# Optimization experiments

Measured on AMD Instinct MI355X. Metric: run time of the kernel, lower is better.

The kernel has to match this reference:

```python
import jax, jax.numpy as jnp
import numpy as np

B, N, C = 2, 2048, 1024
H = 16
HD = C // H
GH = C // 4  # spatial gate hidden dim


def setup_inputs() -> dict:
    key = jax.random.key(0)
    ks = jax.random.split(key, 10)
    s = 0.02
    return {
        "x": jax.random.normal(ks[0], (B, N, C), dtype=jnp.float32),
        "spatial_mask": jax.random.uniform(ks[1], (B, N), dtype=jnp.float32),
        # qkv Linear: weight [3C, C], bias [3C] (torch convention: y = x @ W.T + b)
        "qkv_w": jax.random.normal(ks[2], (3 * C, C), dtype=jnp.float32) * s,
        "qkv_b": jnp.zeros((3 * C,), dtype=jnp.float32),
        # output proj Linear: weight [C, C], bias [C]
        "proj_w": jax.random.normal(ks[3], (C, C), dtype=jnp.float32) * s,
        "proj_b": jnp.zeros((C,), dtype=jnp.float32),
        # spatial_gate: Linear(1, C//4) -> ReLU -> Linear(C//4, 1) -> Sigmoid
        "g1_w": jax.random.normal(ks[4], (GH, 1), dtype=jnp.float32) * 0.5,
        "g1_b": jnp.zeros((GH,), dtype=jnp.float32),
        "g2_w": jax.random.normal(ks[5], (1, GH), dtype=jnp.float32) * 0.1,
        "g2_b": jnp.zeros((1,), dtype=jnp.float32),
    }


def reference(x, spatial_mask, qkv_w, qkv_b, proj_w, proj_b, g1_w, g1_b, g2_w, g2_b):
    b, n, c = x.shape
    # QKV projection: [B, N, 3C] -> [3, B, H, N, HD]
    qkv = (x @ qkv_w.T + qkv_b).reshape(b, n, 3, H, HD).transpose(2, 0, 3, 1, 4)
    q, k, v = qkv[0], qkv[1], qkv[2]

    # scaled attention scores [B, H, N, N]
    attn = jnp.einsum("bhqd,bhkd->bhqk", q, k) * (HD ** -0.5)

    # spatial gate on the mask: scalar MLP applied per key position
    m = spatial_mask[..., None]                      # [B, N, 1]
    h = jax.nn.relu(m @ g1_w.T + g1_b)               # [B, N, GH]
    gate = jax.nn.sigmoid(h @ g2_w.T + g2_b)         # [B, N, 1]
    gate = gate[:, None, None, :, 0]                 # [B, 1, 1, N] broadcasts over heads & queries

    attn = jax.nn.softmax(attn * gate, axis=-1)

    out = jnp.einsum("bhqk,bhkd->bhqd", attn, v)     # [B, H, N, HD]
    out = out.transpose(0, 2, 1, 3).reshape(b, n, c) # [B, N, C]
    return out @ proj_w.T + proj_b
```

## Files before the change

### kernel.cpp

```cpp
#include <hip/hip_runtime.h>

#define H 16
#define NSEQ 2048
#define HD 64
#define CDIM 1024

typedef __attribute__((ext_vector_type(8))) short s8v;
typedef __attribute__((ext_vector_type(4))) float f4v;

#define GLL(g, l) __builtin_amdgcn_global_load_lds( \
    (const __attribute__((address_space(1))) void*)(g), \
    (__attribute__((address_space(3))) void*)(l), 16, 0, 0)

__device__ __forceinline__ short f2bf(float f) {
  union { float f; unsigned u; } x; x.f = f;
  unsigned r = (x.u + 0x7fffu + ((x.u >> 16) & 1u)) >> 16;
  return (short)r;
}

__global__ __launch_bounds__(256) void cvt_kernel(const float* __restrict__ in,
                                                  short* __restrict__ out, int n4) {
  int i = blockIdx.x * 256 + threadIdx.x;
  if (i < n4) {
    float4 f = ((const float4*)in)[i];
    short4 s;
    s.x = f2bf(f.x); s.y = f2bf(f.y); s.z = f2bf(f.z); s.w = f2bf(f.w);
    ((short4*)out)[i] = s;
  }
}

__global__ __launch_bounds__(256) void gate_kernel(const float* __restrict__ mask,
    const float* __restrict__ g1w, const float* __restrict__ g1b,
    const float* __restrict__ g2w, const float* __restrict__ g2b,
    float* __restrict__ gate) {
  int i = blockIdx.x * 256 + threadIdx.x;
  float m = mask[i];
  float acc = 0.f;
  for (int j = 0; j < 256; j++) {
    float h = m * g1w[j] + g1b[j];
    h = fmaxf(h, 0.f);
    acc += g2w[j] * h;
  }
  gate[i] = 1.f / (1.f + __expf(-(acc + g2b[0])));
}

__global__ __launch_bounds__(256) void gemm_qkv(const short* __restrict__ X,
    const short* __restrict__ W, const float* __restrict__ bias,
    short* __restrict__ qws, short* __restrict__ kws, short* __restrict__ vtws) {
  __shared__ __align__(16) short At[4096];
  __shared__ __align__(16) short Bt[4096];
  const int K = CDIM;
  int tid = threadIdx.x;
  int lane = tid & 63, w = tid >> 6;
  int quad = lane >> 4, l15 = lane & 15;
  int wm = w >> 1, wn = w & 1;
  long rowBase = (long)blockIdx.y * 128;
  long colBase = (long)blockIdx.x * 128;
  const f4v fz = {0.f, 0.f, 0.f, 0.f};
  f4v acc[4][4];
#pragma unroll
  for (int i = 0; i < 4; i++)
#pragma unroll
    for (int j = 0; j < 4; j++) acc[i][j] = fz;

  int j0 = tid, j1 = 256 + tid;
  int sr0 = j0 >> 2, sp0 = j0 & 3, sc0 = sp0 ^ ((sr0 >> 1) & 3);
  int sr1 = j1 >> 2, sp1 = j1 & 3, sc1 = sp1 ^ ((sr1 >> 1) & 3);
  const short* Xa = X + (rowBase + sr0) * K + sc0 * 8;
  const short* Xb = X + (rowBase + sr1) * K + sc1 * 8;
  const short* Wa = W + (colBase + sr0) * K + sc0 * 8;
  const short* Wb = W + (colBase + sr1) * K + sc1 * 8;

  for (int k0 = 0; k0 < K; k0 += 32) {
    __syncthreads();
    GLL(Xa + k0, &At[j0 * 8]);
    GLL(Xb + k0, &At[j1 * 8]);
    GLL(Wa + k0, &Bt[j0 * 8]);
    GLL(Wb + k0, &Bt[j1 * 8]);
    __syncthreads();
    s8v a[4], b[4];
#pragma unroll
    for (int mi = 0; mi < 4; mi++) {
      int row = wm * 64 + mi * 16 + l15;
      a[mi] = *(const s8v*)&At[row * 32 + ((quad ^ ((row >> 1) & 3)) * 8)];
    }
#pragma unroll
    for (int ni = 0; ni < 4; ni++) {
      int row = wn * 64 + ni * 16 + l15;
      b[ni] = *(const s8v*)&Bt[row * 32 + ((quad ^ ((row >> 1) & 3)) * 8)];
    }
#pragma unroll
    for (int mi = 0; mi < 4; mi++)
#pragma unroll
      for (int ni = 0; ni < 4; ni++)
        acc[mi][ni] = __builtin_amdgcn_mfma_f32_16x16x32_bf16(a[mi], b[ni], acc[mi][ni], 0, 0, 0);
  }
#pragma unroll
  for (int mi = 0; mi < 4; mi++) {
    int row = (int)rowBase + wm * 64 + mi * 16 + quad * 4;
    int bb = row >> 11, nn = row & 2047;
#pragma unroll
    for (int ni = 0; ni < 4; ni++) {
      int col = (int)colBase + wn * 64 + ni * 16 + l15;
      int which = col >> 10, cc = col & 1023;
      int hh = cc >> 6, dd = cc & 63;
      float bcol = bias[col];
      if (which == 2) {
        short4 pv;
        pv.x = f2bf(acc[mi][ni][0] + bcol);
        pv.y = f2bf(acc[mi][ni][1] + bcol);
        pv.z = f2bf(acc[mi][ni][2] + bcol);
        pv.w = f2bf(acc[mi][ni][3] + bcol);
        *(short4*)&vtws[((bb * H + hh) * HD + dd) * NSEQ + nn] = pv;
      } else {
#pragma unroll
        for (int r = 0; r < 4; r++) {
          int idx = ((bb * H + hh) * NSEQ + nn + r) * HD + dd;
          float v = acc[mi][ni][r] + bcol;
          if (which == 0) qws[idx] = f2bf(v * 0.125f);
          else kws[idx] = f2bf(v);
        }
      }
    }
  }
}

__global__ __launch_bounds__(256) void gemm_proj(const short* __restrict__ X,
    const short* __restrict__ W, const float* __restrict__ bias, float* __restrict__ out) {
  __shared__ __align__(16) short At[4096];
  __shared__ __align__(16) short Bt[4096];
  const int K = CDIM;
  int tid = threadIdx.x;
  int lane = tid & 63, w = tid >> 6;
  int quad = lane >> 4, l15 = lane & 15;
  int wm = w >> 1, wn = w & 1;
  long rowBase = (long)blockIdx.y * 128;
  long colBase = (long)blockIdx.x * 128;
  const f4v fz = {0.f, 0.f, 0.f, 0.f};
  f4v acc[4][4];
#pragma unroll
  for (int i = 0; i < 4; i++)
#pragma unroll
    for (int j = 0; j < 4; j++) acc[i][j] = fz;

  int j0 = tid, j1 = 256 + tid;
  int sr0 = j0 >> 2, sp0 = j0 & 3, sc0 = sp0 ^ ((sr0 >> 1) & 3);
  int sr1 = j1 >> 2, sp1 = j1 & 3, sc1 = sp1 ^ ((sr1 >> 1) & 3);
  const short* Xa = X + (rowBase + sr0) * K + sc0 * 8;
  const short* Xb = X + (rowBase + sr1) * K + sc1 * 8;
  const short* Wa = W + (colBase + sr0) * K + sc0 * 8;
  const short* Wb = W + (colBase + sr1) * K + sc1 * 8;

  for (int k0 = 0; k0 < K; k0 += 32) {
    __syncthreads();
    GLL(Xa + k0, &At[j0 * 8]);
    GLL(Xb + k0, &At[j1 * 8]);
    GLL(Wa + k0, &Bt[j0 * 8]);
    GLL(Wb + k0, &Bt[j1 * 8]);
    __syncthreads();
    s8v a[4], b[4];
#pragma unroll
    for (int mi = 0; mi < 4; mi++) {
      int row = wm * 64 + mi * 16 + l15;
      a[mi] = *(const s8v*)&At[row * 32 + ((quad ^ ((row >> 1) & 3)) * 8)];
    }
#pragma unroll
    for (int ni = 0; ni < 4; ni++) {
      int row = wn * 64 + ni * 16 + l15;
      b[ni] = *(const s8v*)&Bt[row * 32 + ((quad ^ ((row >> 1) & 3)) * 8)];
    }
#pragma unroll
    for (int mi = 0; mi < 4; mi++)
#pragma unroll
      for (int ni = 0; ni < 4; ni++)
        acc[mi][ni] = __builtin_amdgcn_mfma_f32_16x16x32_bf16(a[mi], b[ni], acc[mi][ni], 0, 0, 0);
  }
#pragma unroll
  for (int mi = 0; mi < 4; mi++) {
    int row = (int)rowBase + wm * 64 + mi * 16 + quad * 4;
#pragma unroll
    for (int ni = 0; ni < 4; ni++) {
      int col = (int)colBase + wn * 64 + ni * 16 + l15;
      float bcol = bias[col];
#pragma unroll
      for (int r = 0; r < 4; r++)
        out[(long)(row + r) * CDIM + col] = acc[mi][ni][r] + bcol;
    }
  }
}

__global__ __launch_bounds__(256) void attn_kernel(const short* __restrict__ qws,
    const short* __restrict__ kws, const short* __restrict__ vtws,
    const float* __restrict__ gate, short* __restrict__ attn_out) {
  __shared__ __align__(16) short Kt[32][72];
  __shared__ __align__(16) short Vt[80][40];
  __shared__ __align__(16) short Pt[4][16][40];
  int tid = threadIdx.x;
  int lane = tid & 63, w = tid >> 6;
  int quad = lane >> 4, l15 = lane & 15;
  int bh = blockIdx.x >> 5;
  int qt = blockIdx.x & 31;
  int b = bh >> 4, h = bh & 15;
  int qbase = qt * 64;

  if (tid < 160) {
    int rr = tid / 10, ccs = (tid % 10) * 4;
    short val = (rr == 0) ? (short)0x3F80 : (short)0;
    short4 v4; v4.x = val; v4.y = val; v4.z = val; v4.w = val;
    *(short4*)&Vt[64 + rr][ccs] = v4;
  }

  long qoff = ((long)bh * NSEQ + qbase + w * 16 + l15) * HD;
  s8v aq0 = *(const s8v*)&qws[qoff + quad * 8];
  s8v aq1 = *(const s8v*)&qws[qoff + 32 + quad * 8];

  const f4v fz = {0.f, 0.f, 0.f, 0.f};
  f4v o_acc[5];
#pragma unroll
  for (int g = 0; g < 5; g++) o_acc[g] = fz;

  int skey = tid >> 3, scg = (tid & 7) * 8;
  int vd = tid >> 2, vkg = (tid & 3) * 8;
  const short* kbase = kws + ((long)bh * NSEQ + skey) * HD + scg;
  const short* vbase = vtws + (long)bh * HD * NSEQ + vd * NSEQ + vkg;
  const float* gbase = gate + b * NSEQ + l15;

  for (int kb = 0; kb < NSEQ; kb += 32) {
    __syncthreads();
    *(uint4*)&Kt[skey][scg] = *(const uint4*)&kbase[(long)kb * HD];
    *(uint4*)&Vt[vd][vkg]   = *(const uint4*)&vbase[kb];
    __syncthreads();

    float p[2][4];
#pragma unroll
    for (int g = 0; g < 2; g++) {
      s8v bk0 = *(const s8v*)&Kt[g * 16 + l15][quad * 8];
      s8v bk1 = *(const s8v*)&Kt[g * 16 + l15][32 + quad * 8];
      f4v t = __builtin_amdgcn_mfma_f32_16x16x32_bf16(aq0, bk0, fz, 0, 0, 0);
      t = __builtin_amdgcn_mfma_f32_16x16x32_bf16(aq1, bk1, t, 0, 0, 0);
      float gw = gbase[kb + g * 16];
#pragma unroll
      for (int r = 0; r < 4; r++) p[g][r] = __expf(t[r] * gw);
    }

#pragma unroll
    for (int g = 0; g < 2; g++)
#pragma unroll
      for (int r = 0; r < 4; r++)
        Pt[w][quad * 4 + r][g * 16 + l15] = f2bf(p[g][r]);
    s8v ap = *(const s8v*)&Pt[w][l15][quad * 8];

#pragma unroll
    for (int g = 0; g < 5; g++) {
      s8v bv = *(const s8v*)&Vt[g * 16 + l15][quad * 8];
      o_acc[g] = __builtin_amdgcn_mfma_f32_16x16x32_bf16(ap, bv, o_acc[g], 0, 0, 0);
    }
  }

  float inv[4];
#pragma unroll
  for (int r = 0; r < 4; r++) {
    float l = __shfl(o_acc[4][r], quad * 16);
    inv[r] = 1.f / l;
  }
#pragma unroll
  for (int g = 0; g < 4; g++)
#pragma unroll
    for (int r = 0; r < 4; r++) {
      int n = qbase + w * 16 + quad * 4 + r;
      int c = h * HD + g * 16 + l15;
      attn_out[((long)b * NSEQ + n) * CDIM + c] = f2bf(o_acc[g][r] * inv[r]);
    }
}

extern "C" void kernel_launch(void* const* d_in, const int* in_sizes, int n_in,
                              void* d_out, int out_size, void* d_ws, size_t ws_size,
                              hipStream_t stream) {
  const float* x     = (const float*)d_in[0];
  const float* mask  = (const float*)d_in[1];
  const float* qkvw  = (const float*)d_in[2];
  const float* qkvb  = (const float*)d_in[3];
  const float* projw = (const float*)d_in[4];
  const float* projb = (const float*)d_in[5];
  const float* g1w   = (const float*)d_in[6];
  const float* g1b   = (const float*)d_in[7];
  const float* g2w   = (const float*)d_in[8];
  const float* g2b   = (const float*)d_in[9];
  float* out = (float*)d_out;

  char* ws = (char*)d_ws;
  short* x_bf    = (short*)(ws);
  short* w_qkv   = (short*)(ws + 8388608);
  short* w_proj  = (short*)(ws + 14680064);
  short* q_ws    = (short*)(ws + 16777216);
  short* k_ws    = (short*)(ws + 25165824);
  short* vt_ws   = (short*)(ws + 33554432);
  short* attn_bf = (short*)(ws + 41943040);
  float* gate    = (float*)(ws + 50331648);

  cvt_kernel<<<4096, 256, 0, stream>>>(x, x_bf, 1048576);
  cvt_kernel<<<3072, 256, 0, stream>>>(qkvw, w_qkv, 786432);
  cvt_kernel<<<1024, 256, 0, stream>>>(projw, w_proj, 262144);
  gate_kernel<<<16, 256, 0, stream>>>(mask, g1w, g1b, g2w, g2b, gate);

  dim3 gq(24, 32);
  gemm_qkv<<<gq, 256, 0, stream>>>(x_bf, w_qkv, qkvb, q_ws, k_ws, vt_ws);

  attn_kernel<<<1024, 256, 0, stream>>>(q_ws, k_ws, vt_ws, gate, attn_bf);

  dim3 gp(8, 32);
  gemm_proj<<<gp, 256, 0, stream>>>(attn_bf, w_proj, projb, out);
}
```

Before: 256.9 us.

## Rewrite attention with 32x32 MFMA tiles, async LDS loads and gate folded into K

The attention kernel is rebuilt around 128-query tiles, 64-key blocks and 32x32x16 MFMAs. K and V tiles are loaded straight into XOR-swizzled LDS with global_load_lds, and the key range is split across two waves whose partial outputs and row sums are merged through shared memory at the end. The gate and log2(e) are folded into K inside the QKV GEMM epilogue so the inner loop can use a bare exp2, and the three input conversion launches are merged into one. The aim is more MFMA throughput and data reuse and fewer launches, in exchange for more LDS and register pressure and cheaper truncation-style bf16 rounding of P.

```diff
diff --git a/kernel.cpp b/kernel.cpp
--- a/kernel.cpp
+++ b/kernel.cpp
@@ -7,6 +7,7 @@
 
 typedef __attribute__((ext_vector_type(8))) short s8v;
 typedef __attribute__((ext_vector_type(4))) float f4v;
+typedef __attribute__((ext_vector_type(16))) float f16v;
 
 #define GLL(g, l) __builtin_amdgcn_global_load_lds( \
     (const __attribute__((address_space(1))) void*)(g), \
@@ -17,16 +18,27 @@
   unsigned r = (x.u + 0x7fffu + ((x.u >> 16) & 1u)) >> 16;
   return (short)r;
 }
-
-__global__ __launch_bounds__(256) void cvt_kernel(const float* __restrict__ in,
-                                                  short* __restrict__ out, int n4) {
+__device__ __forceinline__ short f2bf_fast(float f) {
+  return (short)((__float_as_uint(f) + 0x8000u) >> 16);
+}
+__device__ __forceinline__ unsigned pk(float a, float b) {
+  unsigned ua = __float_as_uint(a) + 0x8000u;
+  unsigned ub = __float_as_uint(b) + 0x8000u;
+  return __builtin_amdgcn_perm(ub, ua, 0x07060302);
+}
+
+__global__ __launch_bounds__(256) void cvt3_kernel(
+    const float* __restrict__ a, const float* __restrict__ b, const float* __restrict__ c,
+    short* __restrict__ oa, short* __restrict__ ob, short* __restrict__ oc) {
   int i = blockIdx.x * 256 + threadIdx.x;
-  if (i < n4) {
-    float4 f = ((const float4*)in)[i];
-    short4 s;
-    s.x = f2bf(f.x); s.y = f2bf(f.y); s.z = f2bf(f.z); s.w = f2bf(f.w);
-    ((short4*)out)[i] = s;
-  }
+  const float* src; short* dst; int j;
+  if (i < 1048576)      { src = a; dst = oa; j = i; }
+  else if (i < 1835008) { src = b; dst = ob; j = i - 1048576; }
+  else                  { src = c; dst = oc; j = i - 1835008; }
+  float4 f = ((const float4*)src)[j];
+  short4 s;
+  s.x = f2bf(f.x); s.y = f2bf(f.y); s.z = f2bf(f.z); s.w = f2bf(f.w);
+  ((short4*)dst)[j] = s;
 }
 
 __global__ __launch_bounds__(256) void gate_kernel(const float* __restrict__ mask,
@@ -45,7 +57,7 @@
 }
 
 __global__ __launch_bounds__(256) void gemm_qkv(const short* __restrict__ X,
-    const short* __restrict__ W, const float* __restrict__ bias,
+    const short* __restrict__ W, const float* __restrict__ bias, const float* __restrict__ gate,
     short* __restrict__ qws, short* __restrict__ kws, short* __restrict__ vtws) {
   __shared__ __align__(16) short At[4096];
   __shared__ __align__(16) short Bt[4096];
@@ -115,10 +127,11 @@
       } else {
 #pragma unroll
         for (int r = 0; r < 4; r++) {
-          int idx = ((bb * H + hh) * NSEQ + nn + r) * HD + dd;
+          int rw = row + r;
+          int idx = ((bb * H + hh) * NSEQ + (rw & 2047)) * HD + dd;
           float v = acc[mi][ni][r] + bcol;
           if (which == 0) qws[idx] = f2bf(v * 0.125f);
-          else kws[idx] = f2bf(v);
+          else kws[idx] = f2bf(v * (gate[rw] * 1.44269504f));
         }
       }
     }
@@ -189,88 +202,151 @@
   }
 }
 
-__global__ __launch_bounds__(256) void attn_kernel(const short* __restrict__ qws,
+__global__ __launch_bounds__(256, 2) void attn_kernel(const short* __restrict__ qws,
     const short* __restrict__ kws, const short* __restrict__ vtws,
-    const float* __restrict__ gate, short* __restrict__ attn_out) {
-  __shared__ __align__(16) short Kt[32][72];
-  __shared__ __align__(16) short Vt[80][40];
-  __shared__ __align__(16) short Pt[4][16][40];
+    short* __restrict__ attn_out) {
+  __shared__ __align__(16) char smem[36864];
+  short* Kt = (short*)smem;
+  short* Vt = (short*)(smem + 8192);
+  short* Pt = (short*)(smem + 16384);
+  float* oscr = (float*)smem;
+  float* lscr = (float*)(smem + 33792);
+  float* linv = (float*)(smem + 34816);
+
   int tid = threadIdx.x;
   int lane = tid & 63, w = tid >> 6;
-  int quad = lane >> 4, l15 = lane & 15;
-  int bh = blockIdx.x >> 5;
-  int qt = blockIdx.x & 31;
-  int b = bh >> 4, h = bh & 15;
-  int qbase = qt * 64;
-
-  if (tid < 160) {
-    int rr = tid / 10, ccs = (tid % 10) * 4;
-    short val = (rr == 0) ? (short)0x3F80 : (short)0;
-    short4 v4; v4.x = val; v4.y = val; v4.z = val; v4.w = val;
-    *(short4*)&Vt[64 + rr][ccs] = v4;
-  }
-
-  long qoff = ((long)bh * NSEQ + qbase + w * 16 + l15) * HD;
-  s8v aq0 = *(const s8v*)&qws[qoff + quad * 8];
-  s8v aq1 = *(const s8v*)&qws[qoff + 32 + quad * 8];
-
-  const f4v fz = {0.f, 0.f, 0.f, 0.f};
-  f4v o_acc[5];
-#pragma unroll
-  for (int g = 0; g < 5; g++) o_acc[g] = fz;
-
-  int skey = tid >> 3, scg = (tid & 7) * 8;
-  int vd = tid >> 2, vkg = (tid & 3) * 8;
-  const short* kbase = kws + ((long)bh * NSEQ + skey) * HD + scg;
-  const short* vbase = vtws + (long)bh * HD * NSEQ + vd * NSEQ + vkg;
-  const float* gbase = gate + b * NSEQ + l15;
-
-  for (int kb = 0; kb < NSEQ; kb += 32) {
-    __syncthreads();
-    *(uint4*)&Kt[skey][scg] = *(const uint4*)&kbase[(long)kb * HD];
-    *(uint4*)&Vt[vd][vkg]   = *(const uint4*)&vbase[kb];
-    __syncthreads();
-
-    float p[2][4];
-#pragma unroll
-    for (int g = 0; g < 2; g++) {
-      s8v bk0 = *(const s8v*)&Kt[g * 16 + l15][quad * 8];
-      s8v bk1 = *(const s8v*)&Kt[g * 16 + l15][32 + quad * 8];
-      f4v t = __builtin_amdgcn_mfma_f32_16x16x32_bf16(aq0, bk0, fz, 0, 0, 0);
-      t = __builtin_amdgcn_mfma_f32_16x16x32_bf16(aq1, bk1, t, 0, 0, 0);
-      float gw = gbase[kb + g * 16];
-#pragma unroll
-      for (int r = 0; r < 4; r++) p[g][r] = __expf(t[r] * gw);
-    }
-
-#pragma unroll
-    for (int g = 0; g < 2; g++)
-#pragma unroll
-      for (int r = 0; r < 4; r++)
-        Pt[w][quad * 4 + r][g * 16 + l15] = f2bf(p[g][r]);
-    s8v ap = *(const s8v*)&Pt[w][l15][quad * 8];
-
-#pragma unroll
-    for (int g = 0; g < 5; g++) {
-      s8v bv = *(const s8v*)&Vt[g * 16 + l15][quad * 8];
-      o_acc[g] = __builtin_amdgcn_mfma_f32_16x16x32_bf16(ap, bv, o_acc[g], 0, 0, 0);
-    }
-  }
-
-  float inv[4];
-#pragma unroll
-  for (int r = 0; r < 4; r++) {
-    float l = __shfl(o_acc[4][r], quad * 16);
-    inv[r] = 1.f / l;
-  }
-#pragma unroll
-  for (int g = 0; g < 4; g++)
-#pragma unroll
-    for (int r = 0; r < 4; r++) {
-      int n = qbase + w * 16 + quad * 4 + r;
-      int c = h * HD + g * 16 + l15;
-      attn_out[((long)b * NSEQ + n) * CDIM + c] = f2bf(o_acc[g][r] * inv[r]);
-    }
+  int l31 = lane & 31, hf = lane >> 5;
+  int wq = w >> 1, wk = w & 1;
+  int sw = l31 & 7;
+  int bh = blockIdx.x >> 4, qt = blockIdx.x & 15;
+  int b = bh >> 4, head = bh & 15;
+  int qbase = qt * 128;
+
+  s8v qf[2][4];
+  {
+    const short* qp = qws + ((long)bh * NSEQ + qbase + wq * 64 + l31) * HD + hf * 8;
+#pragma unroll
+    for (int rt = 0; rt < 2; rt++)
+#pragma unroll
+      for (int ds = 0; ds < 4; ds++)
+        qf[rt][ds] = *(const s8v*)&qp[rt * 32 * HD + ds * 16];
+  }
+
+  const f16v fz16 = {0.f,0.f,0.f,0.f,0.f,0.f,0.f,0.f,0.f,0.f,0.f,0.f,0.f,0.f,0.f,0.f};
+  f16v oacc[2][2];
+#pragma unroll
+  for (int rt = 0; rt < 2; rt++)
+#pragma unroll
+    for (int nt = 0; nt < 2; nt++) oacc[rt][nt] = fz16;
+  float l_r[2] = {0.f, 0.f};
+
+  int r8 = lane >> 3, c8 = lane & 7;
+  int row0 = w * 16 + r8, row1 = w * 16 + 8 + r8;
+  const short* kg0 = kws + ((long)bh * NSEQ + row0) * HD + (c8 ^ (row0 & 7)) * 8;
+  const short* kg1 = kws + ((long)bh * NSEQ + row1) * HD + (c8 ^ (row1 & 7)) * 8;
+  const short* vg0 = vtws + ((long)bh * HD + row0) * NSEQ + (c8 ^ (row0 & 7)) * 8;
+  const short* vg1 = vtws + ((long)bh * HD + row1) * NSEQ + (c8 ^ (row1 & 7)) * 8;
+  short* kl0 = Kt + (w * 16) * 64;
+  short* kl1 = Kt + (w * 16 + 8) * 64;
+  short* vl0 = Vt + (w * 16) * 64;
+  short* vl1 = Vt + (w * 16 + 8) * 64;
+
+  const short* myKrow = Kt + (wk * 32 + l31) * 64;
+  short* myP0 = Pt + ((w * 2 + 0) * 32 + l31) * 40;
+  short* myP1 = Pt + ((w * 2 + 1) * 32 + l31) * 40;
+
+  for (int kb = 0; kb < NSEQ; kb += 64) {
+    __syncthreads();
+    GLL(kg0 + (long)kb * HD, kl0);
+    GLL(kg1 + (long)kb * HD, kl1);
+    GLL(vg0 + kb, vl0);
+    GLL(vg1 + kb, vl1);
+    __syncthreads();
+
+#pragma unroll
+    for (int rt = 0; rt < 2; rt++) {
+      f16v s = fz16;
+#pragma unroll
+      for (int ds = 0; ds < 4; ds++) {
+        s8v ak = *(const s8v*)&myKrow[((2 * ds + hf) ^ sw) * 8];
+        s = __builtin_amdgcn_mfma_f32_32x32x16_bf16(ak, qf[rt][ds], s, 0, 0, 0);
+      }
+      float p[16];
+#pragma unroll
+      for (int i = 0; i < 16; i++) p[i] = __builtin_amdgcn_exp2f(s[i]);
+      float ls = 0.f;
+#pragma unroll
+      for (int i = 0; i < 16; i++) ls += p[i];
+      ls += __shfl_xor(ls, 32);
+      l_r[rt] += ls;
+      short* myP = rt ? myP1 : myP0;
+#pragma unroll
+      for (int q = 0; q < 4; q++) {
+        uint2 wv;
+        wv.x = pk(p[4 * q], p[4 * q + 1]);
+        wv.y = pk(p[4 * q + 2], p[4 * q + 3]);
+        *(uint2*)&myP[8 * q + 4 * hf] = wv;
+      }
+    }
+#pragma unroll
+    for (int rt = 0; rt < 2; rt++) {
+      short* myP = rt ? myP1 : myP0;
+#pragma unroll
+      for (int ks = 0; ks < 2; ks++) {
+        s8v ap = *(const s8v*)&myP[ks * 16 + hf * 8];
+#pragma unroll
+        for (int nt = 0; nt < 2; nt++) {
+          s8v bv = *(const s8v*)&Vt[(nt * 32 + l31) * 64 + (((4 * wk + 2 * ks + hf) ^ sw) * 8)];
+          oacc[rt][nt] = __builtin_amdgcn_mfma_f32_32x32x16_bf16(ap, bv, oacc[rt][nt], 0, 0, 0);
+        }
+      }
+    }
+  }
+
+  __syncthreads();
+  if (wk == 1) {
+#pragma unroll
+    for (int rt = 0; rt < 2; rt++) {
+      lscr[128 + wq * 64 + rt * 32 + l31] = l_r[rt];
+#pragma unroll
+      for (int nt = 0; nt < 2; nt++)
+#pragma unroll
+        for (int q = 0; q < 4; q++) {
+          f4v t = {oacc[rt][nt][4 * q], oacc[rt][nt][4 * q + 1],
+                   oacc[rt][nt][4 * q + 2], oacc[rt][nt][4 * q + 3]};
+          *(f4v*)&oscr[(nt * 32 + l31) * 132 + wq * 64 + rt * 32 + 8 * q + 4 * hf] = t;
+        }
+    }
+  } else {
+#pragma unroll
+    for (int rt = 0; rt < 2; rt++) lscr[wq * 64 + rt * 32 + l31] = l_r[rt];
+  }
+  __syncthreads();
+  if (wk == 0) {
+#pragma unroll
+    for (int rt = 0; rt < 2; rt++) {
+      float lt = l_r[rt] + lscr[128 + wq * 64 + rt * 32 + l31];
+      linv[wq * 64 + rt * 32 + l31] = __builtin_amdgcn_rcpf(lt);
+    }
+#pragma unroll
+    for (int rt = 0; rt < 2; rt++)
+#pragma unroll
+      for (int nt = 0; nt < 2; nt++) {
+        int c = head * HD + nt * 32 + l31;
+#pragma unroll
+        for (int q = 0; q < 4; q++) {
+          int rowbase = wq * 64 + rt * 32 + 8 * q + 4 * hf;
+          f4v part = *(const f4v*)&oscr[(nt * 32 + l31) * 132 + rowbase];
+          f4v li = *(const f4v*)&linv[rowbase];
+#pragma unroll
+          for (int r = 0; r < 4; r++) {
+            float val = (oacc[rt][nt][4 * q + r] + part[r]) * li[r];
+            int n = qbase + rowbase + r;
+            attn_out[((long)b * NSEQ + n) * CDIM + c] = f2bf_fast(val);
+          }
+        }
+      }
+  }
 }
 
 extern "C" void kernel_launch(void* const* d_in, const int* in_sizes, int n_in,
@@ -298,15 +374,13 @@
   short* attn_bf = (short*)(ws + 41943040);
   float* gate    = (float*)(ws + 50331648);
 
-  cvt_kernel<<<4096, 256, 0, stream>>>(x, x_bf, 1048576);
-  cvt_kernel<<<3072, 256, 0, stream>>>(qkvw, w_qkv, 786432);
-  cvt_kernel<<<1024, 256, 0, stream>>>(projw, w_proj, 262144);
+  cvt3_kernel<<<8192, 256, 0, stream>>>(x, qkvw, projw, x_bf, w_qkv, w_proj);
   gate_kernel<<<16, 256, 0, stream>>>(mask, g1w, g1b, g2w, g2b, gate);
 
   dim3 gq(24, 32);
-  gemm_qkv<<<gq, 256, 0, stream>>>(x_bf, w_qkv, qkvb, q_ws, k_ws, vt_ws);
-
-  attn_kernel<<<1024, 256, 0, stream>>>(q_ws, k_ws, vt_ws, gate, attn_bf);
+  gemm_qkv<<<gq, 256, 0, stream>>>(x_bf, w_qkv, qkvb, gate, q_ws, k_ws, vt_ws);
+
+  attn_kernel<<<512, 256, 0, stream>>>(q_ws, k_ws, vt_ws, attn_bf);
 
   dim3 gp(8, 32);
   gemm_proj<<<gp, 256, 0, stream>>>(attn_bf, w_proj, projb, out);
```

Measured after the change: 239.6 us. 1.07x faster.
